# Optimization experiments

Measured on AMD Instinct MI355X. Metric: run time of the kernel, lower is better.

Reference implementation:

```python
import jax, jax.numpy as jnp
import numpy as np

BIT = 8          # mantissa bits (incl. sign) for both weights and activations
BLK = 32         # block size along channel dim
QMAX = 2.0 ** (BIT - 1) - 1  # 127
EPS_BN = 1e-5


def bfp_quant(x, bit=BIT, blk=BLK):
    """BFPActivation: block-floating-point quantization of activations.
    Channels are grouped in blocks of `blk`; each block shares the exponent of
    its max-magnitude element, mantissas are rounded to `bit` bits (STE)."""
    N, C, H, W = x.shape
    xb = x.reshape(N, C // blk, blk, H, W)
    max_abs = jnp.max(jnp.abs(xb), axis=2, keepdims=True)
    e = jnp.floor(jnp.log2(jnp.maximum(max_abs, 1e-24)))  # shared exponent
    delta = jnp.exp2(e - (bit - 2))                        # quantization step
    q = jnp.clip(jnp.round(xb / delta), -(2.0 ** (bit - 1)), 2.0 ** (bit - 1) - 1) * delta
    q = q.reshape(N, C, H, W)
    return x + jax.lax.stop_gradient(q - x)  # straight-through


def w_quant(w, bit=BIT, blk=BLK):
    """DSConv2d weight quantization: per (out-channel, in-channel-block, kh, kw)
    float scale (KDS) with `bit`-bit integer mantissa (VQK)."""
    O, I, kh, kw = w.shape
    wb = w.reshape(O, I // blk, blk, kh, kw)
    alpha = jnp.maximum(jnp.max(jnp.abs(wb), axis=2, keepdims=True) / QMAX, 1e-24)
    q = (jnp.round(wb / alpha) * alpha).reshape(O, I, kh, kw)
    return w + jax.lax.stop_gradient(q - w)


def conv(x, w, stride=1, padding=0):
    return jax.lax.conv_general_dilated(
        x, w, (stride, stride), [(padding, padding)] * 2,
        dimension_numbers=("NCHW", "OIHW", "NCHW"))


def bn(x, g, b, m, v):
    # inference-mode BatchNorm2d with running stats
    inv = g / jnp.sqrt(v + EPS_BN)
    return x * inv[None, :, None, None] + (b - m * inv)[None, :, None, None]


def setup_inputs() -> dict:
    key = jax.random.key(0)
    ks = jax.random.split(key, 8)
    N, Cin, H, W_ = 64, 512, 28, 28
    width, Cout = 128, 512
    d = {}
    d["x"] = jax.random.normal(ks[0], (N, Cin, H, W_), jnp.float32)
    d["w1"] = jax.random.normal(ks[1], (width, Cin, 1, 1), jnp.float32) / np.sqrt(Cin)
    d["w2"] = jax.random.normal(ks[2], (width, width, 3, 3), jnp.float32) / np.sqrt(width * 9)
    d["w3"] = jax.random.normal(ks[3], (Cout, width, 1, 1), jnp.float32) / np.sqrt(width)
    for i, c in ((1, width), (2, width), (3, Cout)):
        kk = jax.random.split(jax.random.fold_in(key, i), 4)
        d[f"bn{i}_g"] = 1.0 + 0.1 * jax.random.normal(kk[0], (c,), jnp.float32)
        d[f"bn{i}_b"] = 0.1 * jax.random.normal(kk[1], (c,), jnp.float32)
        d[f"bn{i}_m"] = 0.1 * jax.random.normal(kk[2], (c,), jnp.float32)
        d[f"bn{i}_v"] = 0.5 + jax.random.uniform(kk[3], (c,), jnp.float32)
    return d


def reference(x, w1, w2, w3,
              bn1_g, bn1_b, bn1_m, bn1_v,
              bn2_g, bn2_b, bn2_m, bn2_v,
              bn3_g, bn3_b, bn3_m, bn3_v):
    identity = x
    out = conv(x, w_quant(w1))                       # 1x1, C 512->128
    out = bfp_quant(jax.nn.relu(bn(out, bn1_g, bn1_b, bn1_m, bn1_v)))
    out = conv(out, w_quant(w2), stride=1, padding=1)  # 3x3, C 128->128
    out = bfp_quant(jax.nn.relu(bn(out, bn2_g, bn2_b, bn2_m, bn2_v)))
    out = conv(out, w_quant(w3))                     # 1x1, C 128->512
    out = bn(out, bn3_g, bn3_b, bn3_m, bn3_v)
    out = out + identity
    # seq = Sequential(relu, activation2) in the source (final=False)
    out = bfp_quant(jax.nn.relu(out))
    return out
```

## Files before the change

### kernel.cpp

```cpp
#include <hip/hip_runtime.h>
#include <math.h>


#define HW 784
#define WW 28
#define PTOT 50176

typedef short s8v __attribute__((ext_vector_type(8)));
typedef float f4v __attribute__((ext_vector_type(4)));

__device__ __forceinline__ f4v mfma16(s8v a, s8v b, f4v c) {
  return __builtin_amdgcn_mfma_f32_16x16x32_bf16(a, b, c, 0, 0, 0);
}

__device__ __forceinline__ unsigned short f2bf(float f) {
  unsigned u = __float_as_uint(f);
  u += 0x7fffu + ((u >> 16) & 1u);
  return (unsigned short)(u >> 16);
}
__device__ __forceinline__ float bf2f(unsigned short h) {
  return __uint_as_float(((unsigned)h) << 16);
}

__global__ void wq1_kernel(const float* __restrict__ w, unsigned short* __restrict__ wd) {
  int task = blockIdx.x * blockDim.x + threadIdx.x;
  if (task >= 128 * 16) return;
  int cb = task & 15, o = task >> 4;
  const float* src = w + o * 512 + cb * 32;
  float vals[32], mx = 0.f;
#pragma unroll
  for (int j = 0; j < 32; ++j) { vals[j] = src[j]; mx = fmaxf(mx, fabsf(vals[j])); }
  float alpha = fmaxf(__fdiv_rn(mx, 127.0f), 1e-24f);
#pragma unroll
  for (int j = 0; j < 32; ++j) {
    unsigned short q = f2bf(__fmul_rn(rintf(__fdiv_rn(vals[j], alpha)), alpha));
    wd[o * 1024 + (cb * 32 + j) * 2] = q;
    wd[o * 1024 + (cb * 32 + j) * 2 + 1] = q;
  }
}

__global__ void wq2_kernel(const float* __restrict__ w, unsigned short* __restrict__ wd) {
  int task = blockIdx.x * blockDim.x + threadIdx.x;
  if (task >= 128 * 36) return;
  int o = task / 36, rem = task % 36;
  int khw = rem % 9, cb = rem / 9;
  float vals[32], mx = 0.f;
#pragma unroll
  for (int j = 0; j < 32; ++j) {
    vals[j] = w[(o * 128 + cb * 32 + j) * 9 + khw];
    mx = fmaxf(mx, fabsf(vals[j]));
  }
  float alpha = fmaxf(__fdiv_rn(mx, 127.0f), 1e-24f);
#pragma unroll
  for (int j = 0; j < 32; ++j)
    wd[o * 1152 + khw * 128 + cb * 32 + j] =
        f2bf(__fmul_rn(rintf(__fdiv_rn(vals[j], alpha)), alpha));
}

__global__ void wq3_kernel(const float* __restrict__ w, unsigned short* __restrict__ wd) {
  int task = blockIdx.x * blockDim.x + threadIdx.x;
  if (task >= 512 * 4) return;
  int cb = task & 3, o = task >> 2;
  const float* src = w + o * 128 + cb * 32;
  float vals[32], mx = 0.f;
#pragma unroll
  for (int j = 0; j < 32; ++j) { vals[j] = src[j]; mx = fmaxf(mx, fabsf(vals[j])); }
  float alpha = fmaxf(__fdiv_rn(mx, 127.0f), 1e-24f);
#pragma unroll
  for (int j = 0; j < 32; ++j)
    wd[o * 128 + cb * 32 + j] = f2bf(__fmul_rn(rintf(__fdiv_rn(vals[j], alpha)), alpha));
}

__global__ __launch_bounds__(256, 3) void conv1_fused(
    const float* __restrict__ x, const unsigned short* __restrict__ Wq,
    const float* __restrict__ gg, const float* __restrict__ bb,
    const float* __restrict__ mm, const float* __restrict__ vv,
    unsigned short* __restrict__ out16) {
  __shared__ unsigned short As[2][64][72];

  const int t = threadIdx.x;
  const int w = t >> 6, l = t & 63;
  const int col = l & 15, row4 = l >> 4;
  const int P0 = blockIdx.x * 64;
  const int OG = w * 32;
  const int k0 = row4 * 8;

  const int p = P0 + l;
  const int n = p / HW;
  const int hw = p - n * HW;
  const float* xbase = x + (size_t)n * 512 * HW + hw;

  f4v acc[4][2];
#pragma unroll
  for (int pg = 0; pg < 4; ++pg)
#pragma unroll
    for (int og = 0; og < 2; ++og) acc[pg][og] = (f4v){0.f, 0.f, 0.f, 0.f};

  float xr[8];
#pragma unroll
  for (int j = 0; j < 8; ++j) xr[j] = xbase[(w * 8 + j) * HW];

#pragma unroll 2
  for (int s = 0; s < 16; ++s) {
    s8v sv0, sv1;
#pragma unroll
    for (int j = 0; j < 4; ++j) {
      unsigned short hi = f2bf(xr[j]);
      float lo = __fsub_rn(xr[j], bf2f(hi));
      sv0[2 * j] = (short)hi;
      sv0[2 * j + 1] = (short)f2bf(lo);
    }
#pragma unroll
    for (int j = 0; j < 4; ++j) {
      unsigned short hi = f2bf(xr[4 + j]);
      float lo = __fsub_rn(xr[4 + j], bf2f(hi));
      sv1[2 * j] = (short)hi;
      sv1[2 * j + 1] = (short)f2bf(lo);
    }
    *(s8v*)&As[s & 1][l][w * 16] = sv0;
    *(s8v*)&As[s & 1][l][w * 16 + 8] = sv1;
    __syncthreads();
    if (s < 15) {
#pragma unroll
      for (int j = 0; j < 8; ++j) xr[j] = xbase[((s + 1) * 32 + w * 8 + j) * HW];
    }
#pragma unroll
    for (int kk = 0; kk < 2; ++kk) {
      s8v b0 = *(const s8v*)(Wq + (size_t)(OG + col) * 1024 + s * 64 + kk * 32 + k0);
      s8v b1 = *(const s8v*)(Wq + (size_t)(OG + 16 + col) * 1024 + s * 64 + kk * 32 + k0);
#pragma unroll
      for (int pg = 0; pg < 4; ++pg) {
        s8v af = *(const s8v*)&As[s & 1][pg * 16 + col][kk * 32 + k0];
        acc[pg][0] = mfma16(af, b0, acc[pg][0]);
        acc[pg][1] = mfma16(af, b1, acc[pg][1]);
      }
    }
  }

  float inv_[2], ct_[2];
#pragma unroll
  for (int og = 0; og < 2; ++og) {
    int o = OG + og * 16 + col;
    float iv = __fdiv_rn(gg[o], sqrtf(__fadd_rn(vv[o], 1e-5f)));
    inv_[og] = iv;
    ct_[og] = __fsub_rn(bb[o], __fmul_rn(mm[o], iv));
  }
#pragma unroll
  for (int pg = 0; pg < 4; ++pg) {
#pragma unroll
    for (int r = 0; r < 4; ++r) {
      const int px = P0 + pg * 16 + row4 * 4 + r;
      float v0 = __fadd_rn(__fmul_rn(acc[pg][0][r], inv_[0]), ct_[0]);
      float v1 = __fadd_rn(__fmul_rn(acc[pg][1][r], inv_[1]), ct_[1]);
      v0 = fmaxf(v0, 0.f);
      v1 = fmaxf(v1, 0.f);
      float mx = fmaxf(v0, v1);
#pragma unroll
      for (int sfl = 1; sfl < 16; sfl <<= 1) mx = fmaxf(mx, __shfl_xor(mx, sfl));
      mx = fmaxf(mx, 1e-24f);
      int e = (int)(__float_as_uint(mx) >> 23) - 127;
      float dlt = __uint_as_float((unsigned)(e - 6 + 127) << 23);
      float idlt = __uint_as_float((unsigned)(6 - e + 127) << 23);
      float q0 = fminf(fmaxf(rintf(__fmul_rn(v0, idlt)), -128.f), 127.f);
      float q1 = fminf(fmaxf(rintf(__fmul_rn(v1, idlt)), -128.f), 127.f);
      out16[(size_t)px * 128 + OG + col] = f2bf(__fmul_rn(q0, dlt));
      out16[(size_t)px * 128 + OG + 16 + col] = f2bf(__fmul_rn(q1, dlt));
    }
  }
}

#define C2_SETTAP(ty_, tx_)                                                  \
  {                                                                          \
    _Pragma("unroll") for (int pg = 0; pg < 4; ++pg) {                       \
      int h2 = hh[pg] + (ty_)-1, w2 = wl[pg] + (tx_)-1;                      \
      bool ok = ((unsigned)h2 < 28u) & ((unsigned)w2 < 28u);                 \
      ap[pg] = ok ? (A + (size_t)(nb[pg] + h2 * WW + w2) * 128 + k0)         \
                  : (zp + k0);                                               \
    }                                                                        \
  }

#define C2_LOAD(Ab, Bb0, Bb1, s_)                                            \
  {                                                                          \
    const int tap_ = (s_) >> 2, cb_ = (s_)&3;                                \
    if (cb_ == 0) C2_SETTAP(tap_ / 3, tap_ % 3);                             \
    Bb0 = *(const s8v*)(bb0 + tap_ * 128 + cb_ * 32);                        \
    Bb1 = *(const s8v*)(bb1 + tap_ * 128 + cb_ * 32);                        \
    _Pragma("unroll") for (int pg = 0; pg < 4; ++pg)                         \
        Ab[pg] = *(const s8v*)(ap[pg] + cb_ * 32);                           \
  }

#define C2_MFMA(Ab, Bb0, Bb1)                                                \
  {                                                                          \
    _Pragma("unroll") for (int pg = 0; pg < 4; ++pg) {                       \
      acc[pg][0] = mfma16(Ab[pg], Bb0, acc[pg][0]);                          \
      acc[pg][1] = mfma16(Ab[pg], Bb1, acc[pg][1]);                          \
    }                                                                        \
  }

__global__ __launch_bounds__(256, 3) void conv2_im2col(
    const unsigned short* __restrict__ A, const unsigned short* __restrict__ Wq,
    const float* __restrict__ gg, const float* __restrict__ bb,
    const float* __restrict__ mm, const float* __restrict__ vv,
    unsigned short* __restrict__ out16, const unsigned short* __restrict__ zp) {
  const int t = threadIdx.x;
  const int w = t >> 6, l = t & 63;
  const int col = l & 15, row4 = l >> 4;
  const int bid = blockIdx.x;
  const int P0 = ((bid & 7) * 98 + (bid >> 3)) * 64;
  const int OG = w * 32;
  const int k0 = row4 * 8;

  const unsigned short* bb0 = Wq + (size_t)(OG + col) * 1152 + k0;
  const unsigned short* bb1 = Wq + (size_t)(OG + 16 + col) * 1152 + k0;

  f4v acc[4][2];
#pragma unroll
  for (int pg = 0; pg < 4; ++pg)
#pragma unroll
    for (int og = 0; og < 2; ++og) acc[pg][og] = (f4v){0.f, 0.f, 0.f, 0.f};

  int hh[4], wl[4], nb[4];
#pragma unroll
  for (int pg = 0; pg < 4; ++pg) {
    int p = P0 + pg * 16 + col;
    int n = p / HW, hw = p - n * HW;
    hh[pg] = hw / WW;
    wl[pg] = hw - hh[pg] * WW;
    nb[pg] = n * HW;
  }

  const unsigned short* ap[4];
  s8v A0[4], A1[4], B00, B01, B10, B11;
  C2_LOAD(A0, B00, B01, 0);
#pragma unroll
  for (int ss = 0; ss < 18; ++ss) {
    C2_LOAD(A1, B10, B11, 2 * ss + 1);
    C2_MFMA(A0, B00, B01);
    if (ss < 17) C2_LOAD(A0, B00, B01, 2 * ss + 2);
    C2_MFMA(A1, B10, B11);
  }

  float inv_[2], ct_[2];
#pragma unroll
  for (int og = 0; og < 2; ++og) {
    int o = OG + og * 16 + col;
    float iv = __fdiv_rn(gg[o], sqrtf(__fadd_rn(vv[o], 1e-5f)));
    inv_[og] = iv;
    ct_[og] = __fsub_rn(bb[o], __fmul_rn(mm[o], iv));
  }
#pragma unroll
  for (int pg = 0; pg < 4; ++pg) {
#pragma unroll
    for (int r = 0; r < 4; ++r) {
      const int px = P0 + pg * 16 + row4 * 4 + r;
      float v0 = __fadd_rn(__fmul_rn(acc[pg][0][r], inv_[0]), ct_[0]);
      float v1 = __fadd_rn(__fmul_rn(acc[pg][1][r], inv_[1]), ct_[1]);
      v0 = fmaxf(v0, 0.f);
      v1 = fmaxf(v1, 0.f);
      float mx = fmaxf(v0, v1);
#pragma unroll
      for (int sfl = 1; sfl < 16; sfl <<= 1) mx = fmaxf(mx, __shfl_xor(mx, sfl));
      mx = fmaxf(mx, 1e-24f);
      int e = (int)(__float_as_uint(mx) >> 23) - 127;
      float dlt = __uint_as_float((unsigned)(e - 6 + 127) << 23);
      float idlt = __uint_as_float((unsigned)(6 - e + 127) << 23);
      float q0 = fminf(fmaxf(rintf(__fmul_rn(v0, idlt)), -128.f), 127.f);
      float q1 = fminf(fmaxf(rintf(__fmul_rn(v1, idlt)), -128.f), 127.f);
      out16[(size_t)px * 128 + OG + col] = f2bf(__fmul_rn(q0, dlt));
      out16[(size_t)px * 128 + OG + 16 + col] = f2bf(__fmul_rn(q1, dlt));
    }
  }
}

__global__ __launch_bounds__(256) void conv3_res(
    const unsigned short* __restrict__ A, const unsigned short* __restrict__ Wq,
    const float* __restrict__ gg, const float* __restrict__ bb,
    const float* __restrict__ mm, const float* __restrict__ vv,
    const float* __restrict__ resid, float* __restrict__ outf) {
  const int t = threadIdx.x;
  const int w = t >> 6, l = t & 63;
  const int col = l & 15, row4 = l >> 4;
  const int P0 = blockIdx.x * 64;
  const int OG = blockIdx.y * 128 + w * 32;
  const int k0 = row4 * 8;

  const unsigned short* ab[4];
#pragma unroll
  for (int pg = 0; pg < 4; ++pg)
    ab[pg] = A + (size_t)(P0 + pg * 16 + col) * 128 + k0;
  const unsigned short* b0p = Wq + (size_t)(OG + col) * 128 + k0;
  const unsigned short* b1p = Wq + (size_t)(OG + 16 + col) * 128 + k0;

  f4v acc[4][2];
#pragma unroll
  for (int pg = 0; pg < 4; ++pg)
#pragma unroll
    for (int og = 0; og < 2; ++og) acc[pg][og] = (f4v){0.f, 0.f, 0.f, 0.f};

#pragma unroll
  for (int kb = 0; kb < 4; ++kb) {
    s8v bf0 = *(const s8v*)(b0p + kb * 32);
    s8v bf1 = *(const s8v*)(b1p + kb * 32);
#pragma unroll
    for (int pg = 0; pg < 4; ++pg) {
      s8v af = *(const s8v*)(ab[pg] + kb * 32);
      acc[pg][0] = mfma16(af, bf0, acc[pg][0]);
      acc[pg][1] = mfma16(af, bf1, acc[pg][1]);
    }
  }

  float inv_[2], ct_[2];
#pragma unroll
  for (int og = 0; og < 2; ++og) {
    int o = OG + og * 16 + col;
    float iv = __fdiv_rn(gg[o], sqrtf(__fadd_rn(vv[o], 1e-5f)));
    inv_[og] = iv;
    ct_[og] = __fsub_rn(bb[o], __fmul_rn(mm[o], iv));
  }

#pragma unroll
  for (int pg = 0; pg < 4; ++pg) {
    const int px0 = P0 + pg * 16 + row4 * 4;
    const int n = px0 / HW;
    const int hw0 = px0 - n * HW;
    const size_t base0 = ((size_t)n * 512 + OG + col) * HW + hw0;
    const size_t base1 = ((size_t)n * 512 + OG + 16 + col) * HW + hw0;
    const float4 r0 = *(const float4*)(resid + base0);
    const float4 r1 = *(const float4*)(resid + base1);
    const float rr0[4] = {r0.x, r0.y, r0.z, r0.w};
    const float rr1[4] = {r1.x, r1.y, r1.z, r1.w};
    float s0[4], s1[4];
#pragma unroll
    for (int r = 0; r < 4; ++r) {
      float v0 = __fadd_rn(__fmul_rn(acc[pg][0][r], inv_[0]), ct_[0]);
      float v1 = __fadd_rn(__fmul_rn(acc[pg][1][r], inv_[1]), ct_[1]);
      v0 = __fadd_rn(v0, rr0[r]);
      v1 = __fadd_rn(v1, rr1[r]);
      v0 = fmaxf(v0, 0.f);
      v1 = fmaxf(v1, 0.f);
      float mx = fmaxf(v0, v1);
#pragma unroll
      for (int sfl = 1; sfl < 16; sfl <<= 1) mx = fmaxf(mx, __shfl_xor(mx, sfl));
      mx = fmaxf(mx, 1e-24f);
      int e = (int)(__float_as_uint(mx) >> 23) - 127;
      float dlt = __uint_as_float((unsigned)(e - 6 + 127) << 23);
      float idlt = __uint_as_float((unsigned)(6 - e + 127) << 23);
      float q0 = fminf(fmaxf(rintf(__fmul_rn(v0, idlt)), -128.f), 127.f);
      float q1 = fminf(fmaxf(rintf(__fmul_rn(v1, idlt)), -128.f), 127.f);
      s0[r] = __fmul_rn(q0, dlt);
      s1[r] = __fmul_rn(q1, dlt);
    }
    *(float4*)(outf + base0) = make_float4(s0[0], s0[1], s0[2], s0[3]);
    *(float4*)(outf + base1) = make_float4(s1[0], s1[1], s1[2], s1[3]);
  }
}

extern "C" void kernel_launch(void* const* d_in, const int* in_sizes, int n_in,
                              void* d_out, int out_size, void* d_ws, size_t ws_size,
                              hipStream_t stream) {
  (void)in_sizes; (void)n_in; (void)out_size; (void)ws_size;
  const float* x = (const float*)d_in[0];
  const float* w1 = (const float*)d_in[1];
  const float* w2 = (const float*)d_in[2];
  const float* w3 = (const float*)d_in[3];
  const float* bn1g = (const float*)d_in[4];
  const float* bn1b = (const float*)d_in[5];
  const float* bn1m = (const float*)d_in[6];
  const float* bn1v = (const float*)d_in[7];
  const float* bn2g = (const float*)d_in[8];
  const float* bn2b = (const float*)d_in[9];
  const float* bn2m = (const float*)d_in[10];
  const float* bn2v = (const float*)d_in[11];
  const float* bn3g = (const float*)d_in[12];
  const float* bn3b = (const float*)d_in[13];
  const float* bn3m = (const float*)d_in[14];
  const float* bn3v = (const float*)d_in[15];

  unsigned short* ws = (unsigned short*)d_ws;
  unsigned short* zp = ws;
  unsigned short* w1d = ws + 256;
  unsigned short* w2q = w1d + 128 * 1024;
  unsigned short* w3q = w2q + 128 * 1152;
  unsigned short* a1 = w3q + 512 * 128;
  unsigned short* a2 = a1 + (size_t)PTOT * 128;

  hipMemsetAsync(zp, 0, 512, stream);

  wq1_kernel<<<8, 256, 0, stream>>>(w1, w1d);
  wq2_kernel<<<18, 256, 0, stream>>>(w2, w2q);
  wq3_kernel<<<8, 256, 0, stream>>>(w3, w3q);

  conv1_fused<<<dim3(PTOT / 64, 1), 256, 0, stream>>>(
      x, w1d, bn1g, bn1b, bn1m, bn1v, a1);
  conv2_im2col<<<dim3(PTOT / 64, 1), 256, 0, stream>>>(
      a1, w2q, bn2g, bn2b, bn2m, bn2v, a2, zp);
  conv3_res<<<dim3(PTOT / 64, 4), 256, 0, stream>>>(
      a2, w3q, bn3g, bn3b, bn3m, bn3v, x, (float*)d_out);
}
```

Before: 380.6 us.

## Stage conv2 im2col activation tiles into LDS via direct global-to-LDS loads

Conv2 previously had every wave load its own copy of the shared activation rows straight from global memory into registers. Now each 3x3 tap's 64-pixel by 128-channel tile is loaded once per block into double-buffered, XOR-swizzled LDS using global_load_lds. All four waves then read that tile from LDS for their MFMAs, while per-tap weight fragments are prefetched into registers. This cuts redundant global and L2 traffic, at the cost of a block barrier per tap and extra LDS use that may lower occupancy.

```diff
diff --git a/kernel.cpp b/kernel.cpp
--- a/kernel.cpp
+++ b/kernel.cpp
@@ -20,6 +20,12 @@
 }
 __device__ __forceinline__ float bf2f(unsigned short h) {
   return __uint_as_float(((unsigned)h) << 16);
+}
+
+__device__ __forceinline__ void gload_lds16(const void* g, void* l) {
+  __builtin_amdgcn_global_load_lds(
+      (const __attribute__((address_space(1))) unsigned*)g,
+      (__attribute__((address_space(3))) unsigned*)l, 16, 0, 0);
 }
 
 __global__ void wq1_kernel(const float* __restrict__ w, unsigned short* __restrict__ wd) {
@@ -169,39 +175,13 @@
   }
 }
 
-#define C2_SETTAP(ty_, tx_)                                                  \
-  {                                                                          \
-    _Pragma("unroll") for (int pg = 0; pg < 4; ++pg) {                       \
-      int h2 = hh[pg] + (ty_)-1, w2 = wl[pg] + (tx_)-1;                      \
-      bool ok = ((unsigned)h2 < 28u) & ((unsigned)w2 < 28u);                 \
-      ap[pg] = ok ? (A + (size_t)(nb[pg] + h2 * WW + w2) * 128 + k0)         \
-                  : (zp + k0);                                               \
-    }                                                                        \
-  }
-
-#define C2_LOAD(Ab, Bb0, Bb1, s_)                                            \
-  {                                                                          \
-    const int tap_ = (s_) >> 2, cb_ = (s_)&3;                                \
-    if (cb_ == 0) C2_SETTAP(tap_ / 3, tap_ % 3);                             \
-    Bb0 = *(const s8v*)(bb0 + tap_ * 128 + cb_ * 32);                        \
-    Bb1 = *(const s8v*)(bb1 + tap_ * 128 + cb_ * 32);                        \
-    _Pragma("unroll") for (int pg = 0; pg < 4; ++pg)                         \
-        Ab[pg] = *(const s8v*)(ap[pg] + cb_ * 32);                           \
-  }
-
-#define C2_MFMA(Ab, Bb0, Bb1)                                                \
-  {                                                                          \
-    _Pragma("unroll") for (int pg = 0; pg < 4; ++pg) {                       \
-      acc[pg][0] = mfma16(Ab[pg], Bb0, acc[pg][0]);                          \
-      acc[pg][1] = mfma16(Ab[pg], Bb1, acc[pg][1]);                          \
-    }                                                                        \
-  }
-
 __global__ __launch_bounds__(256, 3) void conv2_im2col(
     const unsigned short* __restrict__ A, const unsigned short* __restrict__ Wq,
     const float* __restrict__ gg, const float* __restrict__ bb,
     const float* __restrict__ mm, const float* __restrict__ vv,
     unsigned short* __restrict__ out16, const unsigned short* __restrict__ zp) {
+  __shared__ unsigned short As[2][4][64][32];
+
   const int t = threadIdx.x;
   const int w = t >> 6, l = t & 63;
   const int col = l & 15, row4 = l >> 4;
@@ -210,6 +190,17 @@
   const int OG = w * 32;
   const int k0 = row4 * 8;
 
+  const int spx = t >> 2;
+  const int scp = (t & 3) ^ ((spx >> 1) & 3);
+  const int sp = P0 + spx;
+  const int sn = sp / HW;
+  const int shw = sp - sn * HW;
+  const int sh = shw / WW, sw = shw - (shw / WW) * WW;
+  const size_t nbase = (size_t)sn * HW;
+
+  unsigned short* lds0 = &As[0][0][0][0];
+  unsigned short* ldsw = lds0 + (size_t)w * 512;
+
   const unsigned short* bb0 = Wq + (size_t)(OG + col) * 1152 + k0;
   const unsigned short* bb1 = Wq + (size_t)(OG + 16 + col) * 1152 + k0;
 
@@ -219,25 +210,54 @@
 #pragma unroll
     for (int og = 0; og < 2; ++og) acc[pg][og] = (f4v){0.f, 0.f, 0.f, 0.f};
 
-  int hh[4], wl[4], nb[4];
-#pragma unroll
-  for (int pg = 0; pg < 4; ++pg) {
-    int p = P0 + pg * 16 + col;
-    int n = p / HW, hw = p - n * HW;
-    hh[pg] = hw / WW;
-    wl[pg] = hw - hh[pg] * WW;
-    nb[pg] = n * HW;
-  }
-
-  const unsigned short* ap[4];
-  s8v A0[4], A1[4], B00, B01, B10, B11;
-  C2_LOAD(A0, B00, B01, 0);
-#pragma unroll
-  for (int ss = 0; ss < 18; ++ss) {
-    C2_LOAD(A1, B10, B11, 2 * ss + 1);
-    C2_MFMA(A0, B00, B01);
-    if (ss < 17) C2_LOAD(A0, B00, B01, 2 * ss + 2);
-    C2_MFMA(A1, B10, B11);
+  s8v Bcur[8], Bnxt[8];
+
+#define C2_STAGE(tap_, buf_)                                                 \
+  {                                                                          \
+    const int ty_ = (tap_) / 3, tx_ = (tap_) - ty_ * 3;                      \
+    const int h2_ = sh + ty_ - 1, w2_ = sw + tx_ - 1;                        \
+    const bool ok_ = ((unsigned)h2_ < 28u) & ((unsigned)w2_ < 28u);          \
+    const unsigned short* s0_ =                                              \
+        ok_ ? (A + (nbase + h2_ * WW + w2_) * 128 + scp * 8) : (zp + scp * 8);\
+    _Pragma("unroll") for (int cb = 0; cb < 4; ++cb)                         \
+        gload_lds16(s0_ + cb * 32, ldsw + (buf_)*8192 + cb * 2048);          \
+  }
+
+#define C2_LOADB(tap_, B_)                                                   \
+  {                                                                          \
+    _Pragma("unroll") for (int cb = 0; cb < 4; ++cb) {                       \
+      B_[2 * cb] = *(const s8v*)(bb0 + (tap_)*128 + cb * 32);                \
+      B_[2 * cb + 1] = *(const s8v*)(bb1 + (tap_)*128 + cb * 32);            \
+    }                                                                        \
+  }
+
+  C2_STAGE(0, 0);
+  C2_LOADB(0, Bcur);
+  __syncthreads();
+
+#pragma unroll
+  for (int tap = 0; tap < 9; ++tap) {
+    const int buf = tap & 1;
+    if (tap < 8) {
+      C2_STAGE(tap + 1, buf ^ 1);
+      C2_LOADB(tap + 1, Bnxt);
+    }
+#pragma unroll
+    for (int cb = 0; cb < 4; ++cb) {
+#pragma unroll
+      for (int pg = 0; pg < 4; ++pg) {
+        const int px = pg * 16 + col;
+        const s8v af = *(const s8v*)(lds0 + buf * 8192 + cb * 2048 + px * 32 +
+                                     (row4 ^ ((px >> 1) & 3)) * 8);
+        acc[pg][0] = mfma16(af, Bcur[2 * cb], acc[pg][0]);
+        acc[pg][1] = mfma16(af, Bcur[2 * cb + 1], acc[pg][1]);
+      }
+    }
+    __syncthreads();
+    if (tap < 8) {
+#pragma unroll
+      for (int j = 0; j < 8; ++j) Bcur[j] = Bnxt[j];
+    }
   }
 
   float inv_[2], ct_[2];
```

Measured after the change: 343.2 us. 9.8% less time.
